# Optimization experiments

Hardware: AMD Instinct MI355X
Metric: run time of the kernel (lower is better)

The kernel has to match this reference:

```python
import jax, jax.numpy as jnp
import numpy as np

# tcnn HashGrid config constants
N_LEVELS = 16
F_PER_LEVEL = 2
LOG2_T = 19
T = 1 << LOG2_T          # 524288 entries per level
BASE_RES = 16
PER_LEVEL_SCALE = 2.0
PRIMES = (1, 2654435761)  # tcnn spatial hash primes for 2D

N_POINTS = 4_194_304      # ~2048x2048 pixels


def setup_inputs() -> dict:
    key = jax.random.key(0)
    k1, k2, k3, k4, k5 = jax.random.split(key, 5)
    v_pixel_pos = jax.random.uniform(k1, (N_POINTS, 2), dtype=jnp.float32)
    # tcnn initializes hash grids ~ U(-1e-4, 1e-4); use scaled normals of similar magnitude
    hash_table = jax.random.normal(k2, (N_LEVELS, T, F_PER_LEVEL), dtype=jnp.float32) * 1e-4
    W1 = jax.random.normal(k3, (32, 64), dtype=jnp.float32) * (1.0 / np.sqrt(32).astype(np.float32))
    W2 = jax.random.normal(k4, (64, 64), dtype=jnp.float32) * (1.0 / np.sqrt(64).astype(np.float32))
    W3 = jax.random.normal(k5, (64, 3), dtype=jnp.float32) * (1.0 / np.sqrt(64).astype(np.float32))
    return {"v_pixel_pos": v_pixel_pos, "hash_table": hash_table, "W1": W1, "W2": W2, "W3": W3}


def _hashgrid_encode(pos, table):
    """Multiresolution hash-grid encoding, 2D bilinear. pos: [N,2] in [0,1]; table: [L,T,F]. -> [N, L*F]"""
    feats = []
    for lvl in range(N_LEVELS):  # small fixed loop over levels (structurally distinct resolutions)
        scale = BASE_RES * (PER_LEVEL_SCALE ** lvl) - 1.0
        res = int(np.ceil(scale)) + 1
        p = pos * jnp.float32(scale) + 0.5
        pf = jnp.floor(p)
        w = p - pf                       # bilinear weights, [N,2]
        pi = pf.astype(jnp.uint32)       # base corner, [N,2]
        dense = res * res <= T           # tcnn uses dense indexing when the grid fits
        acc = jnp.zeros((pos.shape[0], F_PER_LEVEL), dtype=table.dtype)
        for dx, dy in ((0, 0), (1, 0), (0, 1), (1, 1)):
            cx = pi[:, 0] + jnp.uint32(dx)
            cy = pi[:, 1] + jnp.uint32(dy)
            if dense:
                idx = cx + cy * jnp.uint32(res)
            else:
                idx = (cx * jnp.uint32(PRIMES[0])) ^ (cy * jnp.uint32(PRIMES[1]))
                idx = idx & jnp.uint32(T - 1)
            wx = w[:, 0] if dx else (1.0 - w[:, 0])
            wy = w[:, 1] if dy else (1.0 - w[:, 1])
            acc = acc + (wx * wy)[:, None] * table[lvl, idx.astype(jnp.int32)]
        feats.append(acc)
    return jnp.concatenate(feats, axis=-1)  # [N, 32]


def reference(v_pixel_pos, hash_table, W1, W2, W3):
    h = _hashgrid_encode(v_pixel_pos, hash_table)   # [N, 32]
    h = jax.nn.relu(h @ W1)                          # [N, 64]
    h = jax.nn.relu(h @ W2)                          # [N, 64]
    return h @ W3                                    # [N, 3], no output activation
```

## Files before the change

### kernel.cpp

```cpp
#include <hip/hip_runtime.h>
#include <hip/hip_fp16.h>


constexpr unsigned TSIZE  = 1u << 19;
constexpr unsigned PRIME2 = 2654435761u;
constexpr int N_HASHED    = 10;
constexpr int LVL0_HASH   = 6;
#define FEAT_SCALE   4096.0f
#define INV_SCALE    (1.0f / 4096.0f)

typedef _Float16 f16x8 __attribute__((ext_vector_type(8)));
typedef float    f32x4 __attribute__((ext_vector_type(4)));
typedef unsigned u32x2 __attribute__((ext_vector_type(2)));
typedef unsigned u32x4 __attribute__((ext_vector_type(4)));

__device__ __forceinline__ unsigned pkh2(float a, float b) {
    __half2 h = __floats2half2_rn(a, b);
    unsigned u; __builtin_memcpy(&u, &h, 4); return u;
}

__device__ __forceinline__ float2 h2f(unsigned u) {
    __half2 h; __builtin_memcpy(&h, &u, 4);
    return __half22float2(h);
}

__global__ __launch_bounds__(256)
void cvt_table(const float* __restrict__ src, unsigned* __restrict__ dst, int n2)
{
    int t = blockIdx.x * blockDim.x + threadIdx.x;
    if (t >= n2) return;
    f32x4 v = __builtin_nontemporal_load((const f32x4*)src + t);
    u32x2 pk;
    pk.x = pkh2(v.x * FEAT_SCALE, v.y * FEAT_SCALE);
    pk.y = pkh2(v.z * FEAT_SCALE, v.w * FEAT_SCALE);
    __builtin_nontemporal_store(pk, (u32x2*)dst + t);
}

__device__ __forceinline__ unsigned hash_feat(float px, float py, float scale,
                                              const unsigned* __restrict__ tblu)
{
    float pxs = fmaf(px, scale, 0.5f);
    float pys = fmaf(py, scale, 0.5f);
    float fx = floorf(pxs), fy = floorf(pys);
    float wx = pxs - fx,   wy = pys - fy;
    unsigned x0 = (unsigned)fx, y0 = (unsigned)fy;

    unsigned hy0 = y0 * PRIME2;
    unsigned hy1 = hy0 + PRIME2;
    unsigned i00 = (x0 ^ hy0) & (TSIZE - 1u);
    unsigned i01 = (x0 ^ hy1) & (TSIZE - 1u);

    unsigned u00, u10, u01, u11;
    if ((x0 & 1u) == 0u) {
        u32x2 pa = *(const u32x2*)(tblu + (i00 & ~1u));
        u32x2 pb = *(const u32x2*)(tblu + (i01 & ~1u));
        u00 = (i00 & 1u) ? pa.y : pa.x;
        u10 = (i00 & 1u) ? pa.x : pa.y;
        u01 = (i01 & 1u) ? pb.y : pb.x;
        u11 = (i01 & 1u) ? pb.x : pb.y;
    } else {
        unsigned i10 = ((x0 + 1u) ^ hy0) & (TSIZE - 1u);
        unsigned i11 = ((x0 + 1u) ^ hy1) & (TSIZE - 1u);
        u00 = tblu[i00];
        u10 = tblu[i10];
        u01 = tblu[i01];
        u11 = tblu[i11];
    }

    float2 c00 = h2f(u00), c10 = h2f(u10), c01 = h2f(u01), c11 = h2f(u11);

    float w00 = (1.0f - wx) * (1.0f - wy);
    float w10 = wx * (1.0f - wy);
    float w01 = (1.0f - wx) * wy;
    float w11 = wx * wy;

    float f0 = w00 * c00.x + w10 * c10.x + w01 * c01.x + w11 * c11.x;
    float f1 = w00 * c00.y + w10 * c10.y + w01 * c01.y + w11 * c11.y;

    return pkh2(f0, f1);
}

__global__ __launch_bounds__(256)
void encode_level(const float* __restrict__ pos,
                  const unsigned* __restrict__ tblu,
                  u32x2* __restrict__ feat,
                  int nhalf, unsigned res)
{
    int t = blockIdx.x * blockDim.x + threadIdx.x;
    if (t >= nhalf) return;
    f32x4 p = __builtin_nontemporal_load((const f32x4*)pos + t);
    float scale = (float)res - 1.0f;
    unsigned a = hash_feat(p.x, p.y, scale, tblu);
    unsigned b = hash_feat(p.z, p.w, scale, tblu);
    u32x2 pk = {a, b};
    __builtin_nontemporal_store(pk, feat + t);
}

__device__ __forceinline__ unsigned dense_feat(float px, float py, float scale,
                                               unsigned res,
                                               const unsigned* __restrict__ tblu)
{
    float pxs = fmaf(px, scale, 0.5f);
    float pys = fmaf(py, scale, 0.5f);
    float fx = floorf(pxs), fy = floorf(pys);
    float wx = pxs - fx,   wy = pys - fy;
    unsigned x0 = (unsigned)fx, y0 = (unsigned)fy;
    unsigned i00 = x0 + y0 * res;
    unsigned i01 = i00 + res;

    unsigned u00, u10, u01, u11;
    if ((x0 & 1u) == 0u) {
        u32x2 pa = *(const u32x2*)(tblu + i00);
        u32x2 pb = *(const u32x2*)(tblu + i01);
        u00 = pa.x; u10 = pa.y;
        u01 = pb.x; u11 = pb.y;
    } else {
        u00 = tblu[i00];
        u10 = tblu[i00 + 1u];
        u01 = tblu[i01];
        u11 = tblu[i01 + 1u];
    }

    float2 c00 = h2f(u00), c10 = h2f(u10), c01 = h2f(u01), c11 = h2f(u11);

    float w00 = (1.0f - wx) * (1.0f - wy);
    float w10 = wx * (1.0f - wy);
    float w01 = (1.0f - wx) * wy;
    float w11 = wx * wy;

    float f0 = w00 * c00.x + w10 * c10.x + w01 * c01.x + w11 * c11.x;
    float f1 = w00 * c00.y + w10 * c10.y + w01 * c01.y + w11 * c11.y;

    return pkh2(f0, f1);
}

__global__ __launch_bounds__(256)
void encode_dense(const float* __restrict__ pos,
                  const unsigned* __restrict__ tbl16,
                  unsigned* __restrict__ feats,
                  int nhalf, int n)
{
    int t = blockIdx.x * blockDim.x + threadIdx.x;
    if (t >= nhalf) return;
    f32x4 p = __builtin_nontemporal_load((const f32x4*)pos + t);
#pragma unroll
    for (int lvl = 0; lvl < 6; lvl++) {
        const unsigned res = 16u << lvl;
        const float scale = (float)res - 1.0f;
        const unsigned* tbl_l = tbl16 + (size_t)lvl * TSIZE;
        unsigned a = dense_feat(p.x, p.y, scale, res, tbl_l);
        unsigned b = dense_feat(p.z, p.w, scale, res, tbl_l);
        u32x2 pk = {a, b};
        __builtin_nontemporal_store(pk, (u32x2*)(feats + (size_t)lvl * n) + t);
    }
}

#define S0B 80
#define S1B 144

__global__ __launch_bounds__(256)
void mlp_mfma16(const unsigned* __restrict__ feats,
                const float* __restrict__ W1,
                const float* __restrict__ W2,
                const float* __restrict__ W3,
                float* __restrict__ out, int n)
{
    __shared__ uint4 lds[4 * 9216 / 16];
    const int lane = threadIdx.x & 63;
    const int wid  = threadIdx.x >> 6;
    const int m    = lane & 15;
    const int q    = lane >> 4;
    char* buf = (char*)lds + wid * 9216;

    f16x8 A1[4];
#pragma unroll
    for (int ft = 0; ft < 4; ft++)
#pragma unroll
        for (int j = 0; j < 8; j++)
            A1[ft][j] = (_Float16)W1[(q * 8 + j) * 64 + ft * 16 + m];

    f16x8 A2[4][2];
#pragma unroll
    for (int ft = 0; ft < 4; ft++)
#pragma unroll
        for (int kb = 0; kb < 2; kb++)
#pragma unroll
            for (int j = 0; j < 8; j++)
                A2[ft][kb][j] = (_Float16)W2[(kb * 32 + q * 8 + j) * 64 + ft * 16 + m];

    f16x8 A3[2];
#pragma unroll
    for (int kb = 0; kb < 2; kb++)
#pragma unroll
        for (int j = 0; j < 8; j++)
            A3[kb][j] = (m < 3) ? (_Float16)W3[(kb * 32 + q * 8 + j) * 3 + m]
                                : (_Float16)0.f;

    const int ntiles  = n >> 6;
    const int wstride = gridDim.x * 4;
    const int niter   = (ntiles + wstride - 1) / wstride;

    for (int it = 0; it < niter; it++) {
        const int t = blockIdx.x * 4 + wid + it * wstride;
        const bool active = (t < ntiles);
        const int p0 = t << 6;
        const int p  = p0 + lane;

        if (active) {
            unsigned fl[16];
#pragma unroll
            for (int l = 0; l < 16; l++)
                fl[l] = __builtin_nontemporal_load(feats + (size_t)l * (size_t)n + p);

            volatile u32x4* w = (volatile u32x4*)(buf + lane * S0B);
            u32x4 w0 = {fl[0],  fl[1],  fl[2],  fl[3]};
            u32x4 w1 = {fl[4],  fl[5],  fl[6],  fl[7]};
            u32x4 w2 = {fl[8],  fl[9],  fl[10], fl[11]};
            u32x4 w3 = {fl[12], fl[13], fl[14], fl[15]};
            w[0] = w0; w[1] = w1; w[2] = w2; w[3] = w3;
        }
        __syncthreads();

        f16x8 B1[4];
        if (active) {
#pragma unroll
            for (int pt = 0; pt < 4; pt++)
                B1[pt] = *(volatile const f16x8*)(buf + (pt * 16 + m) * S0B + q * 16);
        }
        __syncthreads();

        if (active) {
#pragma unroll
            for (int ft = 0; ft < 4; ft++) {
#pragma unroll
                for (int pt = 0; pt < 4; pt++) {
                    f32x4 acc = {0.f, 0.f, 0.f, 0.f};
                    acc = __builtin_amdgcn_mfma_f32_16x16x32_f16(A1[ft], B1[pt], acc, 0, 0, 0);
                    u32x2 pk = {pkh2(fmaxf(acc[0], 0.f), fmaxf(acc[1], 0.f)),
                                pkh2(fmaxf(acc[2], 0.f), fmaxf(acc[3], 0.f))};
                    *(volatile u32x2*)(buf + (pt * 16 + m) * S1B + (ft * 16 + q * 4) * 2) = pk;
                }
            }
        }
        __syncthreads();

        f16x8 B2[4][2];
        if (active) {
#pragma unroll
            for (int pt = 0; pt < 4; pt++)
#pragma unroll
                for (int kb = 0; kb < 2; kb++)
                    B2[pt][kb] = *(volatile const f16x8*)(buf + (pt * 16 + m) * S1B + kb * 64 + q * 16);
        }
        __syncthreads();

        if (active) {
#pragma unroll
            for (int ft = 0; ft < 4; ft++) {
#pragma unroll
                for (int pt = 0; pt < 4; pt++) {
                    f32x4 acc = {0.f, 0.f, 0.f, 0.f};
                    acc = __builtin_amdgcn_mfma_f32_16x16x32_f16(A2[ft][0], B2[pt][0], acc, 0, 0, 0);
                    acc = __builtin_amdgcn_mfma_f32_16x16x32_f16(A2[ft][1], B2[pt][1], acc, 0, 0, 0);
                    u32x2 pk = {pkh2(fmaxf(acc[0], 0.f), fmaxf(acc[1], 0.f)),
                                pkh2(fmaxf(acc[2], 0.f), fmaxf(acc[3], 0.f))};
                    *(volatile u32x2*)(buf + (pt * 16 + m) * S1B + (ft * 16 + q * 4) * 2) = pk;
                }
            }
        }
        __syncthreads();

        if (active) {
            f16x8 B3[4][2];
#pragma unroll
            for (int pt = 0; pt < 4; pt++)
#pragma unroll
                for (int kb = 0; kb < 2; kb++)
                    B3[pt][kb] = *(volatile const f16x8*)(buf + (pt * 16 + m) * S1B + kb * 64 + q * 16);

#pragma unroll
            for (int pt = 0; pt < 4; pt++) {
                f32x4 acc = {0.f, 0.f, 0.f, 0.f};
                acc = __builtin_amdgcn_mfma_f32_16x16x32_f16(A3[0], B3[pt][0], acc, 0, 0, 0);
                acc = __builtin_amdgcn_mfma_f32_16x16x32_f16(A3[1], B3[pt][1], acc, 0, 0, 0);
                if (q == 0) {
                    int po = p0 + pt * 16 + m;
                    out[3 * po + 0] = acc[0] * INV_SCALE;
                    out[3 * po + 1] = acc[1] * INV_SCALE;
                    out[3 * po + 2] = acc[2] * INV_SCALE;
                }
            }
        }
        __syncthreads();
    }
}

__global__ __launch_bounds__(256)
void mlp_mfma(const float* __restrict__ pos,
              const float* __restrict__ table,
              const unsigned* __restrict__ feats,
              const float* __restrict__ W1,
              const float* __restrict__ W2,
              const float* __restrict__ W3,
              float* __restrict__ out, int n)
{
    __shared__ uint4 lds[4 * 9216 / 16];
    const int lane = threadIdx.x & 63;
    const int wid  = threadIdx.x >> 6;
    const int m    = lane & 15;
    const int q    = lane >> 4;
    char* buf = (char*)lds + wid * 9216;

    f16x8 A1[4];
#pragma unroll
    for (int ft = 0; ft < 4; ft++)
#pragma unroll
        for (int j = 0; j < 8; j++)
            A1[ft][j] = (_Float16)W1[(q * 8 + j) * 64 + ft * 16 + m];

    f16x8 A2[4][2];
#pragma unroll
    for (int ft = 0; ft < 4; ft++)
#pragma unroll
        for (int kb = 0; kb < 2; kb++)
#pragma unroll
            for (int j = 0; j < 8; j++)
                A2[ft][kb][j] = (_Float16)W2[(kb * 32 + q * 8 + j) * 64 + ft * 16 + m];

    f16x8 A3[2];
#pragma unroll
    for (int kb = 0; kb < 2; kb++)
#pragma unroll
        for (int j = 0; j < 8; j++)
            A3[kb][j] = (m < 3) ? (_Float16)W3[(kb * 32 + q * 8 + j) * 3 + m]
                                : (_Float16)0.f;

    const int ntiles  = n >> 6;
    const int wstride = gridDim.x * 4;
    const int niter   = (ntiles + wstride - 1) / wstride;

    for (int it = 0; it < niter; it++) {
        const int t = blockIdx.x * 4 + wid + it * wstride;
        const bool active = (t < ntiles);
        const int p0 = t << 6;
        const int p  = p0 + lane;

        if (active) {
            unsigned fl[16];
            float px = pos[2 * p], py = pos[2 * p + 1];
#pragma unroll
            for (int lvl = 0; lvl < 6; lvl++) {
                const unsigned res = 16u << lvl;
                const float scale = (float)res - 1.0f;
                float pxs = fmaf(px, scale, 0.5f);
                float pys = fmaf(py, scale, 0.5f);
                float fx = floorf(pxs), fy = floorf(pys);
                float wx = pxs - fx,   wy = pys - fy;
                unsigned x0 = (unsigned)fx, y0 = (unsigned)fy;
                unsigned i00 = x0 + y0 * res;
                const float* tl = table + (size_t)lvl * (size_t)TSIZE * 2u;
                float2 t00 = *(const float2*)(tl + 2u * i00);
                float2 t10 = *(const float2*)(tl + 2u * (i00 + 1u));
                float2 t01 = *(const float2*)(tl + 2u * (i00 + res));
                float2 t11 = *(const float2*)(tl + 2u * (i00 + res + 1u));
                float w00 = (1.0f - wx) * (1.0f - wy);
                float w10 = wx * (1.0f - wy);
                float w01 = (1.0f - wx) * wy;
                float w11 = wx * wy;
                float f0 = fmaf(w00, t00.x, fmaf(w10, t10.x, fmaf(w01, t01.x, w11 * t11.x)));
                float f1 = fmaf(w00, t00.y, fmaf(w10, t10.y, fmaf(w01, t01.y, w11 * t11.y)));
                fl[lvl] = pkh2(f0 * FEAT_SCALE, f1 * FEAT_SCALE);
            }
#pragma unroll
            for (int l = 0; l < N_HASHED; l++)
                fl[6 + l] = feats[(size_t)l * (size_t)n + p];

            volatile u32x4* w = (volatile u32x4*)(buf + lane * S0B);
            u32x4 w0 = {fl[0],  fl[1],  fl[2],  fl[3]};
            u32x4 w1 = {fl[4],  fl[5],  fl[6],  fl[7]};
            u32x4 w2 = {fl[8],  fl[9],  fl[10], fl[11]};
            u32x4 w3 = {fl[12], fl[13], fl[14], fl[15]};
            w[0] = w0; w[1] = w1; w[2] = w2; w[3] = w3;
        }
        __syncthreads();

        f16x8 B1[4];
        if (active) {
#pragma unroll
            for (int pt = 0; pt < 4; pt++)
                B1[pt] = *(volatile const f16x8*)(buf + (pt * 16 + m) * S0B + q * 16);
        }
        __syncthreads();

        if (active) {
#pragma unroll
            for (int ft = 0; ft < 4; ft++) {
#pragma unroll
                for (int pt = 0; pt < 4; pt++) {
                    f32x4 acc = {0.f, 0.f, 0.f, 0.f};
                    acc = __builtin_amdgcn_mfma_f32_16x16x32_f16(A1[ft], B1[pt], acc, 0, 0, 0);
                    u32x2 pk = {pkh2(fmaxf(acc[0], 0.f), fmaxf(acc[1], 0.f)),
                                pkh2(fmaxf(acc[2], 0.f), fmaxf(acc[3], 0.f))};
                    *(volatile u32x2*)(buf + (pt * 16 + m) * S1B + (ft * 16 + q * 4) * 2) = pk;
                }
            }
        }
        __syncthreads();

        f16x8 B2[4][2];
        if (active) {
#pragma unroll
            for (int pt = 0; pt < 4; pt++)
#pragma unroll
                for (int kb = 0; kb < 2; kb++)
                    B2[pt][kb] = *(volatile const f16x8*)(buf + (pt * 16 + m) * S1B + kb * 64 + q * 16);
        }
        __syncthreads();

        if (active) {
#pragma unroll
            for (int ft = 0; ft < 4; ft++) {
#pragma unroll
                for (int pt = 0; pt < 4; pt++) {
                    f32x4 acc = {0.f, 0.f, 0.f, 0.f};
                    acc = __builtin_amdgcn_mfma_f32_16x16x32_f16(A2[ft][0], B2[pt][0], acc, 0, 0, 0);
                    acc = __builtin_amdgcn_mfma_f32_16x16x32_f16(A2[ft][1], B2[pt][1], acc, 0, 0, 0);
                    u32x2 pk = {pkh2(fmaxf(acc[0], 0.f), fmaxf(acc[1], 0.f)),
                                pkh2(fmaxf(acc[2], 0.f), fmaxf(acc[3], 0.f))};
                    *(volatile u32x2*)(buf + (pt * 16 + m) * S1B + (ft * 16 + q * 4) * 2) = pk;
                }
            }
        }
        __syncthreads();

        if (active) {
            f16x8 B3[4][2];
#pragma unroll
            for (int pt = 0; pt < 4; pt++)
#pragma unroll
                for (int kb = 0; kb < 2; kb++)
                    B3[pt][kb] = *(volatile const f16x8*)(buf + (pt * 16 + m) * S1B + kb * 64 + q * 16);

#pragma unroll
            for (int pt = 0; pt < 4; pt++) {
                f32x4 acc = {0.f, 0.f, 0.f, 0.f};
                acc = __builtin_amdgcn_mfma_f32_16x16x32_f16(A3[0], B3[pt][0], acc, 0, 0, 0);
                acc = __builtin_amdgcn_mfma_f32_16x16x32_f16(A3[1], B3[pt][1], acc, 0, 0, 0);
                if (q == 0) {
                    int po = p0 + pt * 16 + m;
                    out[3 * po + 0] = acc[0] * INV_SCALE;
                    out[3 * po + 1] = acc[1] * INV_SCALE;
                    out[3 * po + 2] = acc[2] * INV_SCALE;
                }
            }
        }
        __syncthreads();
    }
}

__global__ __launch_bounds__(256, 2)
void ngp_mono(const float* __restrict__ pos, const float* __restrict__ table,
              const float* __restrict__ W1, const float* __restrict__ W2,
              const float* __restrict__ W3, float* __restrict__ out, int n)
{
    int i = blockIdx.x * blockDim.x + threadIdx.x;
    if (i >= n) return;
    float px = pos[2 * i], py = pos[2 * i + 1];
    float h1[64];
#pragma unroll
    for (int j = 0; j < 64; j++) h1[j] = 0.0f;
#pragma unroll
    for (int lvl = 0; lvl < 16; lvl++) {
        const unsigned res = 16u << lvl;
        const float scale = (float)res - 1.0f;
        float pxs = fmaf(px, scale, 0.5f);
        float pys = fmaf(py, scale, 0.5f);
        float fx = floorf(pxs), fy = floorf(pys);
        float wx = pxs - fx, wy = pys - fy;
        unsigned x0 = (unsigned)fx, y0 = (unsigned)fy;
        unsigned i00, i10, i01, i11;
        if ((unsigned long long)res * (unsigned long long)res <= (unsigned long long)TSIZE) {
            i00 = x0 + y0 * res; i10 = i00 + 1u; i01 = i00 + res; i11 = i01 + 1u;
        } else {
            unsigned hy0 = y0 * PRIME2, hy1 = (y0 + 1u) * PRIME2;
            i00 = (x0 ^ hy0) & (TSIZE - 1u);
            i10 = ((x0 + 1u) ^ hy0) & (TSIZE - 1u);
            i01 = (x0 ^ hy1) & (TSIZE - 1u);
            i11 = ((x0 + 1u) ^ hy1) & (TSIZE - 1u);
        }
        const float* tl = table + (size_t)lvl * (size_t)TSIZE * 2u;
        float2 t00 = *(const float2*)(tl + 2u * i00);
        float2 t10 = *(const float2*)(tl + 2u * i10);
        float2 t01 = *(const float2*)(tl + 2u * i01);
        float2 t11 = *(const float2*)(tl + 2u * i11);
        float w00 = (1.0f - wx) * (1.0f - wy);
        float w10 = wx * (1.0f - wy);
        float w01 = (1.0f - wx) * wy;
        float w11 = wx * wy;
        float f0 = fmaf(w00, t00.x, fmaf(w10, t10.x, fmaf(w01, t01.x, w11 * t11.x)));
        float f1 = fmaf(w00, t00.y, fmaf(w10, t10.y, fmaf(w01, t01.y, w11 * t11.y)));
        const float* w1r0 = W1 + (2 * lvl) * 64;
        const float* w1r1 = W1 + (2 * lvl + 1) * 64;
#pragma unroll
        for (int j = 0; j < 64; j++)
            h1[j] = fmaf(f0, w1r0[j], fmaf(f1, w1r1[j], h1[j]));
    }
#pragma unroll
    for (int j = 0; j < 64; j++) h1[j] = fmaxf(h1[j], 0.0f);
    float h2[64];
#pragma unroll
    for (int j = 0; j < 64; j++) h2[j] = 0.0f;
#pragma unroll
    for (int k = 0; k < 64; k++) {
        float a = h1[k];
        const float* wr = W2 + k * 64;
#pragma unroll
        for (int j = 0; j < 64; j++) h2[j] = fmaf(a, wr[j], h2[j]);
    }
#pragma unroll
    for (int j = 0; j < 64; j++) h2[j] = fmaxf(h2[j], 0.0f);
    float o0 = 0.0f, o1 = 0.0f, o2 = 0.0f;
#pragma unroll
    for (int k = 0; k < 64; k++) {
        float a = h2[k];
        o0 = fmaf(a, W3[k * 3 + 0], o0);
        o1 = fmaf(a, W3[k * 3 + 1], o1);
        o2 = fmaf(a, W3[k * 3 + 2], o2);
    }
    out[3 * i + 0] = o0; out[3 * i + 1] = o1; out[3 * i + 2] = o2;
}

extern "C" void kernel_launch(void* const* d_in, const int* in_sizes, int n_in,
                              void* d_out, int out_size, void* d_ws, size_t ws_size,
                              hipStream_t stream) {
    const float* pos   = (const float*)d_in[0];
    const float* table = (const float*)d_in[1];
    const float* W1    = (const float*)d_in[2];
    const float* W2    = (const float*)d_in[3];
    const float* W3    = (const float*)d_in[4];
    float* out = (float*)d_out;

    int n = in_sizes[0] / 2;

    size_t tbl16_all   = 16ull * TSIZE * 4u;
    size_t feats16_all = 16ull * (size_t)n * 4u;
    if (ws_size >= tbl16_all + feats16_all && !(n & 511)) {
        unsigned* tbl16 = (unsigned*)d_ws;
        unsigned* feats = (unsigned*)((char*)d_ws + tbl16_all);

        {
            int n2 = (16 * TSIZE) / 2;
            hipLaunchKernelGGL(cvt_table, dim3((n2 + 255) / 256), dim3(256), 0, stream,
                               table, tbl16, n2);
        }
        int nhalf = n / 2;
        {
            hipLaunchKernelGGL(encode_dense, dim3((nhalf + 255) / 256), dim3(256), 0, stream,
                               pos, tbl16, feats, nhalf, n);
        }
        {
            int blocks = (nhalf + 255) / 256;
            for (int l = 0; l < N_HASHED; l++) {
                const unsigned* tbl_l = tbl16 + (size_t)(LVL0_HASH + l) * TSIZE;
                u32x2* feat_l = (u32x2*)(feats + (size_t)(LVL0_HASH + l) * (size_t)n);
                unsigned res = 16u << (l + LVL0_HASH);
                hipLaunchKernelGGL(encode_level, dim3(blocks), dim3(256), 0, stream,
                                   pos, tbl_l, feat_l, nhalf, res);
            }
        }
        {
            hipLaunchKernelGGL(mlp_mfma16, dim3(1024), dim3(256), 0, stream,
                               feats, W1, W2, W3, out, n);
        }
        return;
    }

    size_t tbl16_bytes = (size_t)N_HASHED * TSIZE * 4u;
    size_t feats_bytes = (size_t)N_HASHED * (size_t)n * 4u;
    if (ws_size >= tbl16_bytes + feats_bytes && !(n & 511)) {
        unsigned* tbl16 = (unsigned*)d_ws;
        __half2* feats  = (__half2*)((char*)d_ws + tbl16_bytes);

        {
            int n2 = (N_HASHED * TSIZE) / 2;
            hipLaunchKernelGGL(cvt_table, dim3((n2 + 255) / 256), dim3(256), 0, stream,
                               table + (size_t)LVL0_HASH * TSIZE * 2u, tbl16, n2);
        }
        {
            int nhalf = n / 2;
            int blocks = (nhalf + 255) / 256;
            for (int l = 0; l < N_HASHED; l++) {
                const unsigned* tbl_l = tbl16 + (size_t)l * TSIZE;
                u32x2* feat_l = (u32x2*)(feats + (size_t)l * (size_t)n);
                unsigned res = 16u << (l + LVL0_HASH);
                hipLaunchKernelGGL(encode_level, dim3(blocks), dim3(256), 0, stream,
                                   pos, tbl_l, feat_l, nhalf, res);
            }
        }
        {
            hipLaunchKernelGGL(mlp_mfma, dim3(1024), dim3(256), 0, stream,
                               pos, table, (const unsigned*)feats, W1, W2, W3, out, n);
        }
        return;
    }

    {
        int blocks = (n + 255) / 256;
        hipLaunchKernelGGL(ngp_mono, dim3(blocks), dim3(256), 0, stream,
                           pos, table, W1, W2, W3, out, n);
    }
}
```

Before: 868.8 us.

## Process points in two halves to shrink the intermediate feature buffer

The launcher now splits the points into two halves and runs the encode kernels and the MLP kernel once per half, reusing a feature buffer half the previous size. The aim is for the fp16 feature intermediate (about 128 MB for the full set, 64 MB per half) to stay resident in the last-level cache between the encode write and the MLP read, cutting DRAM traffic. In exchange it doubles the number of kernel launches and adds tail and drain effects at each half boundary. It also tightens the divisibility requirement on n so each half stays aligned.

After: 898.8 us. 1.03x slower.

```diff
diff --git a/kernel.cpp b/kernel.cpp
--- a/kernel.cpp
+++ b/kernel.cpp
@@ -138,7 +138,7 @@
 void encode_dense(const float* __restrict__ pos,
                   const unsigned* __restrict__ tbl16,
                   unsigned* __restrict__ feats,
-                  int nhalf, int n)
+                  int nhalf, int npts)
 {
     int t = blockIdx.x * blockDim.x + threadIdx.x;
     if (t >= nhalf) return;
@@ -151,7 +151,7 @@
         unsigned a = dense_feat(p.x, p.y, scale, res, tbl_l);
         unsigned b = dense_feat(p.z, p.w, scale, res, tbl_l);
         u32x2 pk = {a, b};
-        __builtin_nontemporal_store(pk, (u32x2*)(feats + (size_t)lvl * n) + t);
+        __builtin_nontemporal_store(pk, (u32x2*)(feats + (size_t)lvl * npts) + t);
     }
 }
 
@@ -163,7 +163,7 @@
                 const float* __restrict__ W1,
                 const float* __restrict__ W2,
                 const float* __restrict__ W3,
-                float* __restrict__ out, int n)
+                float* __restrict__ out, int npts)
 {
     __shared__ uint4 lds[4 * 9216 / 16];
     const int lane = threadIdx.x & 63;
@@ -196,7 +196,7 @@
             A3[kb][j] = (m < 3) ? (_Float16)W3[(kb * 32 + q * 8 + j) * 3 + m]
                                 : (_Float16)0.f;
 
-    const int ntiles  = n >> 6;
+    const int ntiles  = npts >> 6;
     const int wstride = gridDim.x * 4;
     const int niter   = (ntiles + wstride - 1) / wstride;
 
@@ -210,7 +210,7 @@
             unsigned fl[16];
 #pragma unroll
             for (int l = 0; l < 16; l++)
-                fl[l] = __builtin_nontemporal_load(feats + (size_t)l * (size_t)n + p);
+                fl[l] = __builtin_nontemporal_load(feats + (size_t)l * (size_t)npts + p);
 
             volatile u32x4* w = (volatile u32x4*)(buf + lane * S0B);
             u32x4 w0 = {fl[0],  fl[1],  fl[2],  fl[3]};
@@ -542,9 +542,10 @@
 
     int n = in_sizes[0] / 2;
 
-    size_t tbl16_all   = 16ull * TSIZE * 4u;
-    size_t feats16_all = 16ull * (size_t)n * 4u;
-    if (ws_size >= tbl16_all + feats16_all && !(n & 511)) {
+    size_t tbl16_all = 16ull * TSIZE * 4u;
+    int np2 = n / 2;
+    size_t feats_half = 16ull * (size_t)np2 * 4u;
+    if (ws_size >= tbl16_all + feats_half && !(n & 1023)) {
         unsigned* tbl16 = (unsigned*)d_ws;
         unsigned* feats = (unsigned*)((char*)d_ws + tbl16_all);
 
@@ -553,24 +554,22 @@
             hipLaunchKernelGGL(cvt_table, dim3((n2 + 255) / 256), dim3(256), 0, stream,
                                table, tbl16, n2);
         }
-        int nhalf = n / 2;
-        {
-            hipLaunchKernelGGL(encode_dense, dim3((nhalf + 255) / 256), dim3(256), 0, stream,
-                               pos, tbl16, feats, nhalf, n);
-        }
-        {
-            int blocks = (nhalf + 255) / 256;
+        int nhalf = np2 / 2;
+        int eblocks = (nhalf + 255) / 256;
+        for (int h = 0; h < 2; h++) {
+            const float* pos_h = pos + 2ull * (size_t)h * (size_t)np2;
+            float* out_h = out + 3ull * (size_t)h * (size_t)np2;
+            hipLaunchKernelGGL(encode_dense, dim3(eblocks), dim3(256), 0, stream,
+                               pos_h, tbl16, feats, nhalf, np2);
             for (int l = 0; l < N_HASHED; l++) {
                 const unsigned* tbl_l = tbl16 + (size_t)(LVL0_HASH + l) * TSIZE;
-                u32x2* feat_l = (u32x2*)(feats + (size_t)(LVL0_HASH + l) * (size_t)n);
+                u32x2* feat_l = (u32x2*)(feats + (size_t)(LVL0_HASH + l) * (size_t)np2);
                 unsigned res = 16u << (l + LVL0_HASH);
-                hipLaunchKernelGGL(encode_level, dim3(blocks), dim3(256), 0, stream,
-                                   pos, tbl_l, feat_l, nhalf, res);
-            }
-        }
-        {
+                hipLaunchKernelGGL(encode_level, dim3(eblocks), dim3(256), 0, stream,
+                                   pos_h, tbl_l, feat_l, nhalf, res);
+            }
             hipLaunchKernelGGL(mlp_mfma16, dim3(1024), dim3(256), 0, stream,
-                               feats, W1, W2, W3, out, n);
+                               feats, W1, W2, W3, out_h, np2);
         }
         return;
     }
```
